# Optimization experiments

Hardware: AMD Instinct MI355X
Metric: run time of the kernel (lower is better)

The kernel has to match this reference:

```python
import jax, jax.numpy as jnp
import numpy as np

B, T, D_MODEL, D_K = 4, 4096, 1024, 64

def setup_inputs() -> dict:
    key = jax.random.key(0)
    k1, k2, k3, k4, k5 = jax.random.split(key, 5)
    x = jax.random.normal(k1, (B, T, D_MODEL), dtype=jnp.float32)
    # rotary freqs_cis as (real, imag) pairs: unit-magnitude like real RoPE
    theta = 10000.0
    inv = 1.0 / (theta ** (jnp.arange(0, D_K, 2, dtype=jnp.float32) / D_K))  # [D_K//2]
    ang = jnp.arange(T, dtype=jnp.float32)[:, None] * inv[None, :]           # [T, D_K//2]
    freqs_cis = jnp.stack([jnp.cos(ang), jnp.sin(ang)], axis=-1)             # [T, D_K//2, 2]
    scale = 1.0 / np.sqrt(D_MODEL)
    Wq = jax.random.normal(k2, (D_MODEL, D_K), dtype=jnp.float32) * scale
    Wk = jax.random.normal(k3, (D_MODEL, D_K), dtype=jnp.float32) * scale
    Wv = jax.random.normal(k4, (D_MODEL, D_K), dtype=jnp.float32) * scale
    return {"x": x, "freqs_cis": freqs_cis, "Wq": Wq, "Wk": Wk, "Wv": Wv}

def _apply_rope(t, fr, fi):
    # t: [B,T,D_K]; fr/fi: [T, D_K//2]. Complex mult on (even, odd) pairs.
    tp = t.reshape(*t.shape[:-1], D_K // 2, 2)       # [B,T,P,2]
    tr, ti = tp[..., 0], tp[..., 1]
    or_ = tr * fr - ti * fi
    oi_ = tr * fi + ti * fr
    return jnp.stack([or_, oi_], axis=-1).reshape(*t.shape[:-1], D_K)

def reference(x, freqs_cis, Wq, Wk, Wv):
    q = x @ Wq                                       # [B,T,D_K]
    k = x @ Wk
    v = x @ Wv
    fr, fi = freqs_cis[..., 0], freqs_cis[..., 1]    # [T, D_K//2]
    q = _apply_rope(q, fr, fi)
    k = _apply_rope(k, fr, fi)
    wei = jnp.einsum('btd,bsd->bts', q, k) * (D_K ** -0.5)   # [B,T,T]
    causal = jnp.tril(jnp.ones((T, T), dtype=bool))
    wei = jnp.where(causal, wei, -jnp.inf)
    wei = jax.nn.softmax(wei, axis=-1)
    return jnp.einsum('bts,bsd->btd', wei, v)        # [B,T,D_K]
```

## Files before the change

### kernel.cpp

```cpp
#include <hip/hip_runtime.h>
#include <hip/hip_bf16.h>

#define BB 4
#define TT 4096
#define DM 1024
#define DK 64
#define NSPLIT 8

using f32x4  = __attribute__((ext_vector_type(4))) float;
using bf16x8 = __attribute__((ext_vector_type(8))) short;

__device__ __forceinline__ short f2bf(float f) {
    __hip_bfloat16 h = __float2bfloat16(f);
    return __builtin_bit_cast(short, h);
}
__device__ __forceinline__ float bf2f(short s) {
    unsigned int u = ((unsigned int)(unsigned short)s) << 16;
    return __builtin_bit_cast(float, u);
}

__global__ __launch_bounds__(256) void wt_kernel(const float* __restrict__ Wq,
                                                 const float* __restrict__ Wk,
                                                 const float* __restrict__ Wv,
                                                 short* __restrict__ Wt) {
    int idx = blockIdx.x * 256 + threadIdx.x;
    if (idx >= 192 * 1024) return;
    int n = idx >> 10;
    int m = idx & 1023;
    const float* W = (n < 64) ? Wq : (n < 128) ? Wk : Wv;
    int c = n & 63;
    Wt[idx] = f2bf(W[m * 64 + c]);
}

__global__ __launch_bounds__(256, 2) void proj_rope(const float* __restrict__ x,
                                                    const float* __restrict__ freqs,
                                                    const short* __restrict__ Wt,
                                                    short* __restrict__ q,
                                                    short* __restrict__ k,
                                                    short* __restrict__ vt)
{
    __shared__ short As[2][2048];
    __shared__ short Bs[2][12288];

    int t  = threadIdx.x;
    int w  = t >> 6;
    int l  = t & 63;
    int lr = l & 15;
    int lg = (l >> 4) & 3;
    int wr = w & 1;
    int wc = w >> 1;
    int bx = blockIdx.x;
    int mt = (bx & 7) * 64 + (bx >> 3);
    int m0 = mt * 32;

    int arow = t >> 3, au = t & 7;
    int aswz = arow & 7;
    int bswz = (t >> 3) & 7;
    const float* gA = x  + (size_t)(m0 + arow) * DM + au * 8;
    const short* gB = Wt + (size_t)(t >> 3) * DM + (t & 7) * 8;

    f32x4 ar[2]; bf16x8 br[6];

#define LOADG(c_) do { int kk = (c_) << 6;                                      \
        ar[0] = *(const f32x4*)(gA + kk);                                       \
        ar[1] = *(const f32x4*)(gA + kk + 4);                                   \
        _Pragma("unroll")                                                       \
        for (int j_ = 0; j_ < 6; ++j_)                                          \
            br[j_] = *(const bf16x8*)(gB + (size_t)(j_ * 32) * DM + kk);        \
    } while (0)

#define WRITELDS(buf_) do {                                                     \
        bf16x8 a0_;                                                             \
        _Pragma("unroll")                                                       \
        for (int j_ = 0; j_ < 4; ++j_) {                                        \
            a0_[j_] = f2bf(ar[0][j_]); a0_[4 + j_] = f2bf(ar[1][j_]);           \
        }                                                                       \
        *(bf16x8*)&As[buf_][arow * 64 + ((au ^ aswz) << 3)] = a0_;              \
        _Pragma("unroll")                                                       \
        for (int j_ = 0; j_ < 6; ++j_)                                          \
            *(bf16x8*)&Bs[buf_][(j_ * 32 + (t >> 3)) * 64 + (((t & 7) ^ bswz) << 3)] = br[j_]; \
    } while (0)

    f32x4 acc[6];
#pragma unroll
    for (int i = 0; i < 6; ++i) acc[i] = (f32x4){0.f, 0.f, 0.f, 0.f};

    LOADG(0); WRITELDS(0); LOADG(1);
    __syncthreads();

    int cur = 0;
    int r7 = lr & 7;
    int amrow = (wr * 16 + lr) * 64;
    for (int ch = 0; ch < 16; ++ch) {
#pragma unroll
        for (int s = 0; s < 2; ++s) {
            int u0 = s * 4 + lg;
            bf16x8 af = *(const bf16x8*)&As[cur][amrow + ((u0 ^ r7) << 3)];
#pragma unroll
            for (int nh = 0; nh < 3; ++nh)
#pragma unroll
                for (int ntl = 0; ntl < 2; ++ntl) {
                    int row = nh * 64 + (wc * 2 + ntl) * 16 + lr;
                    bf16x8 bfr = *(const bf16x8*)&Bs[cur][row * 64 + ((u0 ^ r7) << 3)];
                    acc[nh * 2 + ntl] = __builtin_amdgcn_mfma_f32_16x16x32_bf16(af, bfr, acc[nh * 2 + ntl], 0, 0, 0);
                }
        }
        if (ch + 1 < 16) {
            WRITELDS(cur ^ 1);
            if (ch + 2 < 16) LOADG(ch + 2);
            __syncthreads();
            cur ^= 1;
        }
    }
#undef LOADG
#undef WRITELDS

#pragma unroll
    for (int nh = 0; nh < 2; ++nh) {
        short* dst = nh ? k : q;
        float postscale = nh ? 1.0f : 0.125f;
#pragma unroll
        for (int r = 0; r < 4; ++r) {
            int tg = m0 + wr * 16 + lg * 4 + r;
            int tt = tg & (TT - 1);
#pragma unroll
            for (int ntl = 0; ntl < 2; ++ntl) {
                int c = wc * 32 + ntl * 16 + lr;
                float e = acc[nh * 2 + ntl][r];
                float p = __shfl_xor(e, 1);
                float2 f = ((const float2*)freqs)[(size_t)tt * 32 + (c >> 1)];
                float sgn = (c & 1) ? f.y : -f.y;
                dst[(size_t)tg * DK + c] = f2bf((e * f.x + p * sgn) * postscale);
            }
        }
    }

    __syncthreads();
    short* vs = &As[0][0];
#pragma unroll
    for (int r = 0; r < 4; ++r)
#pragma unroll
        for (int ntl = 0; ntl < 2; ++ntl)
            vs[(wr * 16 + lg * 4 + r) * 64 + wc * 32 + ntl * 16 + lr] = f2bf(acc[4 + ntl][r]);
    __syncthreads();
    int b    = mt >> 7;
    int tt0  = (mt & 127) * 32;
    int c    = t >> 2;
    int tgrp = t & 3;
    bf16x8 v0;
#pragma unroll
    for (int j = 0; j < 8; ++j) v0[j] = vs[(tgrp * 8 + j) * 64 + c];
    *(bf16x8*)(vt + ((size_t)b * DK + c) * TT + tt0 + tgrp * 8) = v0;
}

__global__ __launch_bounds__(256, 4) void attn_kernel(const short* __restrict__ q,
                                                      const short* __restrict__ k,
                                                      const short* __restrict__ vt,
                                                      short* __restrict__ po,
                                                      float* __restrict__ ml)
{
    __shared__ short Kb[64][64];
    __shared__ short Vb[64][64];
    __shared__ short pbuf[4][16][72];

    int w  = threadIdx.x >> 6;
    int l  = threadIdx.x & 63;
    int lr = l & 15;
    int lg = l >> 4;
    int b  = blockIdx.y;
    int s  = blockIdx.z;
    int qt = 63 - blockIdx.x;
    int q0 = qt * 64;
    int qrow_wave = q0 + w * 16;

    const short* qB = q  + (size_t)b * TT * DK;
    const short* kB = k  + (size_t)b * TT * DK;
    const short* vB = vt + (size_t)b * DK * TT;

    bf16x8 qf0 = *(const bf16x8*)(qB + (size_t)(qrow_wave + lr) * DK + 8 * lg);
    bf16x8 qf1 = *(const bf16x8*)(qB + (size_t)(qrow_wave + lr) * DK + 32 + 8 * lg);

    f32x4 of[4];
#pragma unroll
    for (int i = 0; i < 4; ++i) of[i] = (f32x4){0.f, 0.f, 0.f, 0.f};
    float m[4], lsum[4];
#pragma unroll
    for (int r = 0; r < 4; ++r) { m[r] = -INFINITY; lsum[r] = 0.f; }

    int nt = (qt >= s) ? ((qt - s + NSPLIT) >> 3) : 0;

    int srow = threadIdx.x >> 2;
    int u0   = (threadIdx.x & 3) * 2;
    int p0s  = ((u0) ^ (srow & 7)) * 8;
    int p1s  = ((u0 + 1) ^ (srow & 7)) * 8;

    bf16x8 kr0, kr1, vr0, vr1;
    short* mypb = &pbuf[w][0][0];

#define ISSUE(tile_) do {                                                        \
        int kv0_ = (tile_) << 6;                                                 \
        const short* gk_ = kB + (size_t)(kv0_ + srow) * DK + (u0 * 8);           \
        const short* gv_ = vB + (size_t)srow * TT + kv0_ + (u0 * 8);             \
        kr0 = *(const bf16x8*)gk_; kr1 = *(const bf16x8*)(gk_ + 8);              \
        vr0 = *(const bf16x8*)gv_; vr1 = *(const bf16x8*)(gv_ + 8);              \
    } while (0)

#define WRITE() do {                                                             \
        *(bf16x8*)&Kb[srow][p0s] = kr0;                                         \
        *(bf16x8*)&Kb[srow][p1s] = kr1;                                         \
        *(bf16x8*)&Vb[srow][p0s] = vr0;                                         \
        *(bf16x8*)&Vb[srow][p1s] = vr1;                                         \
    } while (0)

    if (nt > 0) {
        ISSUE(s); WRITE();
        if (nt > 1) ISSUE(s + NSPLIT);
        __syncthreads();
        for (int i = 0; i < nt; ++i) {
            int kv0 = (s + i * NSPLIT) << 6;

            f32x4 sc[4];
#pragma unroll
            for (int c = 0; c < 4; ++c) sc[c] = (f32x4){0.f, 0.f, 0.f, 0.f};
#pragma unroll
            for (int c = 0; c < 4; ++c) {
                int row = c * 16 + lr;
                bf16x8 kf0 = *(const bf16x8*)&Kb[row][((lg) ^ (row & 7)) * 8];
                bf16x8 kf1 = *(const bf16x8*)&Kb[row][((4 + lg) ^ (row & 7)) * 8];
                sc[c] = __builtin_amdgcn_mfma_f32_16x16x32_bf16(qf0, kf0, sc[c], 0, 0, 0);
                sc[c] = __builtin_amdgcn_mfma_f32_16x16x32_bf16(qf1, kf1, sc[c], 0, 0, 0);
            }

            if (kv0 == q0) {
#pragma unroll
                for (int r = 0; r < 4; ++r) {
                    int qg = qrow_wave + lg * 4 + r;
#pragma unroll
                    for (int c = 0; c < 4; ++c)
                        sc[c][r] = (kv0 + c * 16 + lr <= qg) ? sc[c][r] : -INFINITY;
                }
            }

            float mx[4];
#pragma unroll
            for (int r = 0; r < 4; ++r)
                mx[r] = fmaxf(fmaxf(sc[0][r], sc[1][r]), fmaxf(sc[2][r], sc[3][r]));
            bool needA = (mx[0] > m[0] + 8.f) || (mx[1] > m[1] + 8.f) ||
                         (mx[2] > m[2] + 8.f) || (mx[3] > m[3] + 8.f);
            if (__any(needA)) {
#pragma unroll
                for (int r = 0; r < 4; ++r) {
                    float t2 = mx[r];
                    t2 = fmaxf(t2, __shfl_xor(t2, 1));
                    t2 = fmaxf(t2, __shfl_xor(t2, 2));
                    t2 = fmaxf(t2, __shfl_xor(t2, 4));
                    t2 = fmaxf(t2, __shfl_xor(t2, 8));
                    float mn = fmaxf(m[r], t2);
                    float alpha = __expf(m[r] - mn);
                    m[r] = mn;
                    lsum[r] *= alpha;
#pragma unroll
                    for (int dt = 0; dt < 4; ++dt) of[dt][r] *= alpha;
                }
            }
#pragma unroll
            for (int r = 0; r < 4; ++r) {
                float p0 = __expf(sc[0][r] - m[r]);
                float p1 = __expf(sc[1][r] - m[r]);
                float p2 = __expf(sc[2][r] - m[r]);
                float p3 = __expf(sc[3][r] - m[r]);
                lsum[r] += (p0 + p1) + (p2 + p3);
                int prow = (lg * 4 + r) * 72;
                mypb[prow + lr]      = f2bf(p0);
                mypb[prow + 16 + lr] = f2bf(p1);
                mypb[prow + 32 + lr] = f2bf(p2);
                mypb[prow + 48 + lr] = f2bf(p3);
            }

#pragma unroll
            for (int ks = 0; ks < 2; ++ks) {
                bf16x8 pa = *(const bf16x8*)(mypb + lr * 72 + ks * 32 + 8 * lg);
#pragma unroll
                for (int dt = 0; dt < 4; ++dt) {
                    int row = dt * 16 + lr;
                    bf16x8 vf = *(const bf16x8*)&Vb[row][((ks * 4 + lg) ^ (row & 7)) * 8];
                    of[dt] = __builtin_amdgcn_mfma_f32_16x16x32_bf16(pa, vf, of[dt], 0, 0, 0);
                }
            }

            if (i + 1 < nt) {
                __syncthreads();
                WRITE();
                if (i + 2 < nt) ISSUE(s + (i + 2) * NSPLIT);
                __syncthreads();
            }
        }
    }
#undef ISSUE
#undef WRITE

#pragma unroll
    for (int r = 0; r < 4; ++r) {
        float ps = lsum[r];
        ps += __shfl_xor(ps, 1);
        ps += __shfl_xor(ps, 2);
        ps += __shfl_xor(ps, 4);
        ps += __shfl_xor(ps, 8);
        lsum[r] = ps;
    }

    short* myo  = po + (((size_t)b * 64 + qt) * NSPLIT + s) * 4096;
    float* myml = ml + (((size_t)b * 64 + qt) * NSPLIT + s) * 128;
#pragma unroll
    for (int r = 0; r < 4; ++r) {
        int row = w * 16 + lg * 4 + r;
#pragma unroll
        for (int dt = 0; dt < 4; ++dt) myo[row * 64 + dt * 16 + lr] = f2bf(of[dt][r]);
        if (lr == 0) { myml[row] = m[r]; myml[64 + row] = lsum[r]; }
    }
}

__global__ __launch_bounds__(256) void merge_kernel(const short* __restrict__ po,
                                                    const float* __restrict__ ml,
                                                    float* __restrict__ out)
{
    int qt = blockIdx.x;
    int b  = blockIdx.y;
    int row = threadIdx.x >> 2;
    int cg  = threadIdx.x & 3;

    size_t mlbase = ((size_t)b * 64 + qt) * NSPLIT * 128;
    float mm[NSPLIT], llv[NSPLIT];
#pragma unroll
    for (int s = 0; s < NSPLIT; ++s) {
        mm[s]  = ml[mlbase + s * 128 + row];
        llv[s] = ml[mlbase + s * 128 + 64 + row];
    }
    float M = -INFINITY;
#pragma unroll
    for (int s = 0; s < NSPLIT; ++s) M = fmaxf(M, mm[s]);
    float e[NSPLIT], den = 0.f;
#pragma unroll
    for (int s = 0; s < NSPLIT; ++s) { e[s] = __expf(mm[s] - M); den += e[s] * llv[s]; }
    float inv = 1.0f / den;

    size_t pbase = ((size_t)b * 64 + qt) * NSPLIT * 4096;
#pragma unroll
    for (int jj = 0; jj < 2; ++jj) {
        int col = cg * 16 + jj * 8;
        float acc8[8];
#pragma unroll
        for (int e2 = 0; e2 < 8; ++e2) acc8[e2] = 0.f;
#pragma unroll
        for (int s = 0; s < NSPLIT; ++s) {
            bf16x8 v = *(const bf16x8*)(po + pbase + s * 4096 + row * 64 + col);
#pragma unroll
            for (int e2 = 0; e2 < 8; ++e2) acc8[e2] += e[s] * bf2f(v[e2]);
        }
        float* orow = out + ((size_t)b * TT + qt * 64 + row) * DK + col;
#pragma unroll
        for (int e2 = 0; e2 < 8; ++e2) orow[e2] = acc8[e2] * inv;
    }
}

extern "C" void kernel_launch(void* const* d_in, const int* in_sizes, int n_in,
                              void* d_out, int out_size, void* d_ws, size_t ws_size,
                              hipStream_t stream) {
    const float* x     = (const float*)d_in[0];
    const float* freqs = (const float*)d_in[1];
    const float* Wq    = (const float*)d_in[2];
    const float* Wk    = (const float*)d_in[3];
    const float* Wv    = (const float*)d_in[4];
    float* out = (float*)d_out;

    char* ws = (char*)d_ws;
    short* Wt  = (short*)ws;
    short* qb  = (short*)(ws + 393216);
    short* kb  = (short*)(ws + 2490368);
    short* vtb = (short*)(ws + 4587520);
    short* po  = (short*)(ws + 6684672);
    float* ml  = (float*)(ws + 23461888);

    hipLaunchKernelGGL(wt_kernel, dim3(768), dim3(256), 0, stream, Wq, Wk, Wv, Wt);
    hipLaunchKernelGGL(proj_rope, dim3(512), dim3(256), 0, stream, x, freqs, Wt, qb, kb, vtb);
    hipLaunchKernelGGL(attn_kernel, dim3(64, BB, NSPLIT), dim3(256), 0, stream, qb, kb, vtb, po, ml);
    hipLaunchKernelGGL(merge_kernel, dim3(64, BB), dim3(256), 0, stream, po, ml, out);
}
```

Before: 60.92 us.

## Load projection weight fragments directly into registers and stage x as fp32 in LDS

The projection kernel no longer stages the weight tile in shared memory. Each lane loads its MFMA B-fragments straight from global memory into double-buffered register sets, with the loop unrolled by two to alternate buffers. The x tile is now kept as fp32 in LDS and converted to bf16 at fragment read time, not at store time. This removes the LDS writes and reads for the weights, at the cost of many more VGPRs, redundant conversion work, and less coalesced global loads of weights that are duplicated across waves.

After: 91.75 us. +50.6%, slower.

```diff
diff --git a/kernel.cpp b/kernel.cpp
--- a/kernel.cpp
+++ b/kernel.cpp
@@ -39,8 +39,7 @@
                                                     short* __restrict__ k,
                                                     short* __restrict__ vt)
 {
-    __shared__ short As[2][2048];
-    __shared__ short Bs[2][12288];
+    __shared__ float As[2][2048];
 
     int t  = threadIdx.x;
     int w  = t >> 6;
@@ -53,67 +52,89 @@
     int mt = (bx & 7) * 64 + (bx >> 3);
     int m0 = mt * 32;
 
-    int arow = t >> 3, au = t & 7;
+    int arow = t >> 3;
+    int au   = (t & 7) * 2;
     int aswz = arow & 7;
-    int bswz = (t >> 3) & 7;
-    const float* gA = x  + (size_t)(m0 + arow) * DM + au * 8;
-    const short* gB = Wt + (size_t)(t >> 3) * DM + (t & 7) * 8;
-
-    f32x4 ar[2]; bf16x8 br[6];
-
-#define LOADG(c_) do { int kk = (c_) << 6;                                      \
-        ar[0] = *(const f32x4*)(gA + kk);                                       \
-        ar[1] = *(const f32x4*)(gA + kk + 4);                                   \
-        _Pragma("unroll")                                                       \
-        for (int j_ = 0; j_ < 6; ++j_)                                          \
-            br[j_] = *(const bf16x8*)(gB + (size_t)(j_ * 32) * DM + kk);        \
-    } while (0)
-
-#define WRITELDS(buf_) do {                                                     \
-        bf16x8 a0_;                                                             \
-        _Pragma("unroll")                                                       \
-        for (int j_ = 0; j_ < 4; ++j_) {                                        \
-            a0_[j_] = f2bf(ar[0][j_]); a0_[4 + j_] = f2bf(ar[1][j_]);           \
-        }                                                                       \
-        *(bf16x8*)&As[buf_][arow * 64 + ((au ^ aswz) << 3)] = a0_;              \
-        _Pragma("unroll")                                                       \
-        for (int j_ = 0; j_ < 6; ++j_)                                          \
-            *(bf16x8*)&Bs[buf_][(j_ * 32 + (t >> 3)) * 64 + (((t & 7) ^ bswz) << 3)] = br[j_]; \
+    const float* gA = x + (size_t)(m0 + arow) * DM + au * 4;
+
+    const short* gb[6];
+#pragma unroll
+    for (int nh = 0; nh < 3; ++nh)
+#pragma unroll
+        for (int ntl = 0; ntl < 2; ++ntl)
+            gb[nh * 2 + ntl] = Wt + (size_t)(nh * 64 + (wc * 2 + ntl) * 16 + lr) * DM + lg * 8;
+
+    f32x4 ar[2];
+    bf16x8 bA[12], bB[12];
+
+#define LOADA(c_) do { int kk = (c_) << 6;                      \
+        ar[0] = *(const f32x4*)(gA + kk);                       \
+        ar[1] = *(const f32x4*)(gA + kk + 4);                   \
+    } while (0)
+
+#define WRITEA(buf_) do {                                                      \
+        *(f32x4*)&As[buf_][arow * 64 + (((au    ) ^ aswz) << 2)] = ar[0];      \
+        *(f32x4*)&As[buf_][arow * 64 + (((au + 1) ^ aswz) << 2)] = ar[1];      \
+    } while (0)
+
+#define LOADB(dst_, c_) do { int kk = (c_) << 6;                               \
+        _Pragma("unroll")                                                      \
+        for (int j_ = 0; j_ < 6; ++j_) {                                       \
+            dst_[j_]     = *(const bf16x8*)(gb[j_] + kk);                      \
+            dst_[6 + j_] = *(const bf16x8*)(gb[j_] + kk + 32);                 \
+        }                                                                      \
     } while (0)
 
     f32x4 acc[6];
 #pragma unroll
     for (int i = 0; i < 6; ++i) acc[i] = (f32x4){0.f, 0.f, 0.f, 0.f};
 
-    LOADG(0); WRITELDS(0); LOADG(1);
-    __syncthreads();
-
-    int cur = 0;
     int r7 = lr & 7;
     int amrow = (wr * 16 + lr) * 64;
-    for (int ch = 0; ch < 16; ++ch) {
-#pragma unroll
-        for (int s = 0; s < 2; ++s) {
-            int u0 = s * 4 + lg;
-            bf16x8 af = *(const bf16x8*)&As[cur][amrow + ((u0 ^ r7) << 3)];
-#pragma unroll
-            for (int nh = 0; nh < 3; ++nh)
-#pragma unroll
-                for (int ntl = 0; ntl < 2; ++ntl) {
-                    int row = nh * 64 + (wc * 2 + ntl) * 16 + lr;
-                    bf16x8 bfr = *(const bf16x8*)&Bs[cur][row * 64 + ((u0 ^ r7) << 3)];
-                    acc[nh * 2 + ntl] = __builtin_amdgcn_mfma_f32_16x16x32_bf16(af, bfr, acc[nh * 2 + ntl], 0, 0, 0);
-                }
-        }
-        if (ch + 1 < 16) {
-            WRITELDS(cur ^ 1);
-            if (ch + 2 < 16) LOADG(ch + 2);
+    int cur = 0;
+
+#define COMPUTE(BS) do {                                                       \
+        _Pragma("unroll")                                                      \
+        for (int s_ = 0; s_ < 2; ++s_) {                                       \
+            int u0_ = s_ * 8 + lg * 2;                                         \
+            f32x4 a0_ = *(const f32x4*)&As[cur][amrow + (((u0_    ) ^ r7) << 2)]; \
+            f32x4 a1_ = *(const f32x4*)&As[cur][amrow + (((u0_ + 1) ^ r7) << 2)]; \
+            bf16x8 af_;                                                        \
+            _Pragma("unroll")                                                  \
+            for (int j_ = 0; j_ < 4; ++j_) { af_[j_] = f2bf(a0_[j_]); af_[4 + j_] = f2bf(a1_[j_]); } \
+            _Pragma("unroll")                                                  \
+            for (int j_ = 0; j_ < 6; ++j_)                                     \
+                acc[j_] = __builtin_amdgcn_mfma_f32_16x16x32_bf16(af_, BS[s_ * 6 + j_], acc[j_], 0, 0, 0); \
+        }                                                                      \
+    } while (0)
+
+    LOADA(0); WRITEA(0);
+    LOADB(bA, 0);
+    LOADA(1);
+    __syncthreads();
+
+#pragma unroll
+    for (int ch = 0; ch < 16; ch += 2) {
+        LOADB(bB, ch + 1);
+        COMPUTE(bA);
+        WRITEA(cur ^ 1);
+        if (ch + 2 < 16) LOADA(ch + 2);
+        __syncthreads();
+        cur ^= 1;
+
+        if (ch + 2 < 16) LOADB(bA, ch + 2);
+        COMPUTE(bB);
+        if (ch + 2 < 16) {
+            WRITEA(cur ^ 1);
+            if (ch + 3 < 16) LOADA(ch + 3);
             __syncthreads();
             cur ^= 1;
         }
     }
-#undef LOADG
-#undef WRITELDS
+#undef LOADA
+#undef WRITEA
+#undef LOADB
+#undef COMPUTE
 
 #pragma unroll
     for (int nh = 0; nh < 2; ++nh) {
@@ -136,7 +157,7 @@
     }
 
     __syncthreads();
-    short* vs = &As[0][0];
+    short* vs = (short*)&As[0][0];
 #pragma unroll
     for (int r = 0; r < 4; ++r)
 #pragma unroll
```
